# Kernel tuning notes

Hardware: AMD Instinct MI355X
Metric: run time of the kernel (lower is better)

## Reference

```python
import jax, jax.numpy as jnp
import numpy as np

N_NODES = 100000
N_EDGES = 1600000
F_IN, H1, H2, N_CLASSES = 512, 64, 32, 16


def setup_inputs() -> dict:
    key = jax.random.key(0)
    ks = jax.random.split(key, 8)
    glorot = lambda k, fi, fo: jax.random.normal(k, (fi, fo), jnp.float32) * (2.0 / (fi + fo)) ** 0.5
    return {
        "x": jax.random.normal(ks[0], (N_NODES, F_IN), jnp.float32),
        "edge_index": jax.random.randint(ks[1], (2, N_EDGES), 0, N_NODES, jnp.int32),
        "W1": glorot(ks[2], F_IN, H1), "b1": jnp.zeros((H1,), jnp.float32),
        "W2": glorot(ks[3], H1, H2), "b2": jnp.zeros((H2,), jnp.float32),
        "W3": glorot(ks[4], H2, N_CLASSES), "b3": jnp.zeros((N_CLASSES,), jnp.float32),
    }


def _gcn_conv(x, W, b, src, dst, norm, n_nodes):
    # GCNConv: D^{-1/2} (A + I) D^{-1/2} X W + b  (transform-then-propagate)
    h = x @ W                                   # [N, out]
    msg = h[src] * norm[:, None]                # gather + scale, [E', out]
    agg = jax.ops.segment_sum(msg, dst, num_segments=n_nodes)  # scatter-add
    return agg + b


def reference(x, edge_index, W1, b1, W2, b2, W3, b3):
    n = x.shape[0]
    loop = jnp.arange(n, dtype=edge_index.dtype)
    src = jnp.concatenate([edge_index[0], loop])  # add self-loops
    dst = jnp.concatenate([edge_index[1], loop])
    deg = jax.ops.segment_sum(jnp.ones_like(src, dtype=x.dtype), dst, num_segments=n)
    dinv = jnp.where(deg > 0, jax.lax.rsqrt(deg), 0.0)
    norm = dinv[src] * dinv[dst]                  # symmetric normalization per edge

    h = jax.nn.relu(_gcn_conv(x, W1, b1, src, dst, norm, n))
    h = jax.nn.relu(_gcn_conv(h, W2, b2, src, dst, norm, n))  # dropout = identity (eval)
    h = _gcn_conv(h, W3, b3, src, dst, norm, n)
    return jax.nn.log_softmax(h, axis=1)
```

## Files before the change

### kernel.cpp

```cpp
#include <hip/hip_runtime.h>
#include <hip/hip_bf16.h>
#include <cstdint>
#include <cstddef>

#define N_NODES 100000
#define N_EDGES 1600000
#define F_IN 512
#define H1F 64
#define H2F 32
#define NCF 16
#define NB 782
#define NBLK 128
#define CHUNK 12500

typedef __attribute__((ext_vector_type(8))) short bf16x8;
typedef __attribute__((ext_vector_type(8))) unsigned short ushort8;
typedef __attribute__((ext_vector_type(4))) float f32x4;

__device__ inline short f2bf(float f) {
    uint32_t u = __builtin_bit_cast(uint32_t, f);
    return (short)((u + 0x7FFF + ((u >> 16) & 1)) >> 16);
}
__device__ inline float bf2f(unsigned short u) {
    uint32_t x = ((uint32_t)u) << 16;
    return __builtin_bit_cast(float, x);
}

__global__ __launch_bounds__(256) void count_kernel(const int* __restrict__ dst,
                                                    int* __restrict__ mat) {
    __shared__ int lh[NB];
    for (int i = threadIdx.x; i < NB; i += 256) lh[i] = 0;
    __syncthreads();
    int base = blockIdx.x * CHUNK;
    for (int j = base + threadIdx.x; j < base + CHUNK; j += 256)
        atomicAdd(&lh[dst[j] >> 7], 1);
    __syncthreads();
    for (int i = threadIdx.x; i < NB; i += 256)
        mat[blockIdx.x * NB + i] = lh[i];
}

__global__ __launch_bounds__(NBLK) void colscan_kernel(int* __restrict__ mat,
                                                       int* __restrict__ total) {
    __shared__ int s[NBLK];
    int b = blockIdx.x;
    int t = threadIdx.x;
    int v = mat[t * NB + b];
    s[t] = v;
    __syncthreads();
    for (int o = 1; o < NBLK; o <<= 1) {
        int a = (t >= o) ? s[t - o] : 0;
        __syncthreads();
        s[t] += a;
        __syncthreads();
    }
    mat[t * NB + b] = s[t] - v;
    if (t == NBLK - 1) total[b] = s[t];
}

__global__ __launch_bounds__(1024) void bscan_kernel(const int* __restrict__ total,
                                                     int* __restrict__ boff,
                                                     int* __restrict__ row_ptr) {
    __shared__ int s[1024];
    int t = threadIdx.x;
    int v = (t < NB) ? total[t] : 0;
    s[t] = v;
    __syncthreads();
    for (int o = 1; o < 1024; o <<= 1) {
        int a = (t >= o) ? s[t - o] : 0;
        __syncthreads();
        s[t] += a;
        __syncthreads();
    }
    if (t < NB) boff[t] = s[t] - v;
    if (t == 0) {
        boff[NB] = N_EDGES;
        row_ptr[N_NODES] = N_EDGES;
    }
}

__global__ __launch_bounds__(256) void place_kernel(const int* __restrict__ src,
                                                    const int* __restrict__ dst,
                                                    const int* __restrict__ boff,
                                                    const int* __restrict__ mat,
                                                    int* __restrict__ ebuf) {
    __shared__ int lcur[NB];
    for (int i = threadIdx.x; i < NB; i += 256)
        lcur[i] = boff[i] + mat[blockIdx.x * NB + i];
    __syncthreads();
    int base = blockIdx.x * CHUNK;
    for (int j = base + threadIdx.x; j < base + CHUNK; j += 256) {
        int d = dst[j];
        int b = d >> 7;
        int pos = atomicAdd(&lcur[b], 1);
        ebuf[pos] = src[j] | ((d & 127) << 17);
    }
}

__global__ __launch_bounds__(256) void bbuild_kernel(const int* __restrict__ ebuf,
                                                     const int* __restrict__ boff,
                                                     int* __restrict__ row_ptr,
                                                     int* __restrict__ col,
                                                     float* __restrict__ dinv) {
    __shared__ int lcnt[128], lexc[128];
    int b = blockIdx.x;
    int beg = boff[b], end = boff[b + 1];
    int t = threadIdx.x;
    if (t < 128) lcnt[t] = 0;
    __syncthreads();
    for (int j = beg + t; j < end; j += 256)
        atomicAdd(&lcnt[(ebuf[j] >> 17) & 127], 1);
    __syncthreads();
    if (t < 128) lexc[t] = lcnt[t];
    __syncthreads();
    for (int o = 1; o < 128; o <<= 1) {
        int a = (t < 128 && t >= o) ? lexc[t - o] : 0;
        __syncthreads();
        if (t < 128) lexc[t] += a;
        __syncthreads();
    }
    int node0 = b << 7;
    if (t < 128) {
        int n = node0 + t;
        if (n < N_NODES) {
            int ex = lexc[t] - lcnt[t];
            row_ptr[n] = beg + ex;
            dinv[n] = rsqrtf((float)(lcnt[t] + 1));
            lexc[t] = ex;
        }
    }
    __syncthreads();
    for (int j = beg + t; j < end; j += 256) {
        int v = ebuf[j];
        int li = (v >> 17) & 127;
        int p = atomicAdd(&lexc[li], 1);
        col[beg + p] = v & 0x1FFFF;
    }
}

__global__ __launch_bounds__(256) void gemm1_mfma(const float* __restrict__ x,
                                                  const float* __restrict__ W,
                                                  const float* __restrict__ dinv,
                                                  unsigned short* __restrict__ out) {
    __shared__ short As[2][4096];
    __shared__ short Bs[2][2048];
    const int tid = threadIdx.x;
    const int L = tid & 63;
    const int w = tid >> 6;
    const int brow = blockIdx.x * 128;

    f32x4 acc[2][4] = {};

    auto stageA = [&](int kt, int buf) {
        #pragma unroll
        for (int h = 0; h < 2; ++h) {
            int r  = (tid >> 2) + h * 64;
            int kg = tid & 3;
            int gr = brow + r;
            float4 v0 = make_float4(0.f, 0.f, 0.f, 0.f);
            float4 v1 = make_float4(0.f, 0.f, 0.f, 0.f);
            if (gr < N_NODES) {
                const float* p = &x[(size_t)gr * F_IN + kt * 32 + kg * 8];
                v0 = *reinterpret_cast<const float4*>(p);
                v1 = *reinterpret_cast<const float4*>(p + 4);
            }
            short t8[8] = {f2bf(v0.x), f2bf(v0.y), f2bf(v0.z), f2bf(v0.w),
                           f2bf(v1.x), f2bf(v1.y), f2bf(v1.z), f2bf(v1.w)};
            *reinterpret_cast<bf16x8*>(&As[buf][kg * 1024 + (r ^ (kg << 2)) * 8]) =
                *reinterpret_cast<bf16x8*>(t8);
        }
    };
    auto stageB = [&](int kt, int buf) {
        int k0 = kt * 32 + w * 8;
        short t8[8];
        #pragma unroll
        for (int i = 0; i < 8; ++i) t8[i] = f2bf(W[(size_t)(k0 + i) * H1F + L]);
        int byteoff = L * 64 + ((w * 16) ^ ((L & 3) << 4));
        *reinterpret_cast<bf16x8*>((char*)Bs[buf] + byteoff) =
            *reinterpret_cast<bf16x8*>(t8);
    };
    auto compute = [&](int buf) {
        const int kg = L >> 4;
        const int lr = L & 15;
        int r0 = w * 32 + lr;
        int r1 = r0 + 16;
        bf16x8 a0 = *reinterpret_cast<bf16x8*>(&As[buf][kg * 1024 + (r0 ^ (kg << 2)) * 8]);
        bf16x8 a1 = *reinterpret_cast<bf16x8*>(&As[buf][kg * 1024 + (r1 ^ (kg << 2)) * 8]);
        #pragma unroll
        for (int ni = 0; ni < 4; ++ni) {
            int c = ni * 16 + lr;
            bf16x8 b = *reinterpret_cast<bf16x8*>(
                (char*)Bs[buf] + c * 64 + ((kg * 16) ^ ((c & 3) << 4)));
            acc[0][ni] = __builtin_amdgcn_mfma_f32_16x16x32_bf16(a0, b, acc[0][ni], 0, 0, 0);
            acc[1][ni] = __builtin_amdgcn_mfma_f32_16x16x32_bf16(a1, b, acc[1][ni], 0, 0, 0);
        }
    };

    stageA(0, 0);
    stageB(0, 0);
    __syncthreads();
    for (int kt = 0; kt < 16; ++kt) {
        int cur = kt & 1;
        if (kt < 15) {
            stageA(kt + 1, cur ^ 1);
            stageB(kt + 1, cur ^ 1);
        }
        compute(cur);
        __syncthreads();
    }

    #pragma unroll
    for (int mi = 0; mi < 2; ++mi) {
        #pragma unroll
        for (int i = 0; i < 4; ++i) {
            int row = brow + w * 32 + mi * 16 + (L >> 4) * 4 + i;
            if (row < N_NODES) {
                float dv = dinv[row];
                #pragma unroll
                for (int ni = 0; ni < 4; ++ni)
                    out[(size_t)row * H1F + ni * 16 + (L & 15)] =
                        (unsigned short)f2bf(acc[mi][ni][i] * dv);
            }
        }
    }
}

__global__ __launch_bounds__(256) void gemm2_kernel(const unsigned short* __restrict__ h,
                                                    const float* __restrict__ W,
                                                    const float* __restrict__ dinv,
                                                    unsigned short* __restrict__ out) {
    __shared__ float ws[64][32];
    __shared__ float rs[8][64];
    int tid = threadIdx.x;
    int brow = blockIdx.x * 8;
    #pragma unroll
    for (int i = 0; i < 2; ++i) {
        int f = tid + i * 256;
        reinterpret_cast<float4*>(&ws[0][0])[f] = reinterpret_cast<const float4*>(W)[f];
    }
    if (tid < 64) {
        ushort8 v = reinterpret_cast<const ushort8*>(h + (size_t)brow * 64)[tid];
        #pragma unroll
        for (int j = 0; j < 8; ++j) (&rs[0][0])[tid * 8 + j] = bf2f(v[j]);
    }
    __syncthreads();
    int lr = tid >> 5;
    int c = tid & 31;
    float acc = 0.f;
    #pragma unroll
    for (int k = 0; k < 64; ++k) acc += rs[lr][k] * ws[k][c];
    int gr = brow + lr;
    out[(size_t)gr * H2F + c] = (unsigned short)f2bf(acc * dinv[gr]);
}

__global__ __launch_bounds__(256) void gemm3_kernel(const unsigned short* __restrict__ h,
                                                    const float* __restrict__ W,
                                                    const float* __restrict__ dinv,
                                                    unsigned short* __restrict__ out) {
    __shared__ float ws[32][16];
    __shared__ float rs[16][32];
    int tid = threadIdx.x;
    int brow = blockIdx.x * 16;
    if (tid < 128) {
        reinterpret_cast<float4*>(&ws[0][0])[tid] = reinterpret_cast<const float4*>(W)[tid];
    } else if (tid < 192) {
        int t = tid - 128;
        ushort8 v = reinterpret_cast<const ushort8*>(h + (size_t)brow * 32)[t];
        #pragma unroll
        for (int j = 0; j < 8; ++j) (&rs[0][0])[t * 8 + j] = bf2f(v[j]);
    }
    __syncthreads();
    int lr = tid >> 4;
    int c = tid & 15;
    float acc = 0.f;
    #pragma unroll
    for (int k = 0; k < 32; ++k) acc += rs[lr][k] * ws[k][c];
    int gr = brow + lr;
    out[(size_t)gr * NCF + c] = (unsigned short)f2bf(acc * dinv[gr]);
}

template <int F, bool RELU, bool LSM>
__global__ __launch_bounds__(256) void aggregate_kernel(const unsigned short* __restrict__ h,
                                                        const int* __restrict__ row_ptr,
                                                        const int* __restrict__ col,
                                                        const float* __restrict__ dinv,
                                                        const float* __restrict__ bias,
                                                        void* __restrict__ outp) {
    int tid = blockIdx.x * 256 + threadIdx.x;
    int n = tid / F;
    int f = tid % F;
    if (n >= N_NODES) return;
    int beg = row_ptr[n];
    int end = row_ptr[n + 1];
    float sum = bf2f(h[(size_t)n * F + f]);
    int j = beg;
    for (; j + 3 < end; j += 4) {
        int c0 = col[j], c1 = col[j + 1], c2 = col[j + 2], c3 = col[j + 3];
        float s0 = bf2f(h[(size_t)c0 * F + f]);
        float s1 = bf2f(h[(size_t)c1 * F + f]);
        float s2 = bf2f(h[(size_t)c2 * F + f]);
        float s3 = bf2f(h[(size_t)c3 * F + f]);
        sum += (s0 + s1) + (s2 + s3);
    }
    for (; j < end; ++j) sum += bf2f(h[(size_t)col[j] * F + f]);

    float val = sum * dinv[n] + bias[f];
    if (RELU) val = fmaxf(val, 0.f);
    if (LSM) {
        float m = val;
        #pragma unroll
        for (int o = 1; o < F; o <<= 1) m = fmaxf(m, __shfl_xor(m, o));
        float ex = expf(val - m);
        float s = ex;
        #pragma unroll
        for (int o = 1; o < F; o <<= 1) s += __shfl_xor(s, o);
        val = val - m - logf(s);
        ((float*)outp)[(size_t)n * F + f] = val;
    } else {
        ((unsigned short*)outp)[(size_t)n * F + f] = (unsigned short)f2bf(val);
    }
}

extern "C" void kernel_launch(void* const* d_in, const int* in_sizes, int n_in,
                              void* d_out, int out_size, void* d_ws, size_t ws_size,
                              hipStream_t stream) {
    const float* x  = (const float*)d_in[0];
    const int*   ei = (const int*)d_in[1];
    const float* W1 = (const float*)d_in[2];
    const float* b1 = (const float*)d_in[3];
    const float* W2 = (const float*)d_in[4];
    const float* b2 = (const float*)d_in[5];
    const float* W3 = (const float*)d_in[6];
    const float* b3 = (const float*)d_in[7];
    float* out = (float*)d_out;

    const int* src = ei;
    const int* dst = ei + N_EDGES;

    char* ws = (char*)d_ws;
    size_t off = 0;
    auto alloc = [&](size_t bytes) -> void* {
        void* p = ws + off;
        off += (bytes + 255) & ~(size_t)255;
        return p;
    };
    int*            row_ptr = (int*)alloc((size_t)(N_NODES + 1) * 4);
    float*          dinv    = (float*)alloc((size_t)N_NODES * 4);
    int*            col     = (int*)alloc((size_t)N_EDGES * 4);
    unsigned short* bufA    = (unsigned short*)alloc((size_t)N_NODES * 64 * 2);
    unsigned short* bufB    = (unsigned short*)alloc((size_t)N_NODES * 64 * 2);
    int*            mat     = (int*)alloc((size_t)NBLK * NB * 4);
    int*            total   = (int*)alloc((size_t)NB * 4);
    int*            boff    = (int*)alloc((size_t)(NB + 1) * 4);
    int*            ebuf    = (int*)bufA;

    count_kernel<<<NBLK, 256, 0, stream>>>(dst, mat);
    colscan_kernel<<<NB, NBLK, 0, stream>>>(mat, total);
    bscan_kernel<<<1, 1024, 0, stream>>>(total, boff, row_ptr);
    place_kernel<<<NBLK, 256, 0, stream>>>(src, dst, boff, mat, ebuf);
    bbuild_kernel<<<NB, 256, 0, stream>>>(ebuf, boff, row_ptr, col, dinv);

    gemm1_mfma<<<(N_NODES + 127) / 128, 256, 0, stream>>>(x, W1, dinv, bufA);
    aggregate_kernel<64, true, false><<<(N_NODES * 64) / 256, 256, 0, stream>>>(
        bufA, row_ptr, col, dinv, b1, bufB);

    gemm2_kernel<<<N_NODES / 8, 256, 0, stream>>>(bufB, W2, dinv, bufA);
    aggregate_kernel<32, true, false><<<(N_NODES * 32) / 256, 256, 0, stream>>>(
        bufA, row_ptr, col, dinv, b2, bufB);

    gemm3_kernel<<<N_NODES / 16, 256, 0, stream>>>(bufB, W3, dinv, bufA);
    aggregate_kernel<16, false, true><<<(N_NODES * 16) / 256, 256, 0, stream>>>(
        bufA, row_ptr, col, dinv, b3, out);
}
```

Measured before the change: 554.5 us.

## Fuse layer-1/2 aggregation with the next layer's small GEMM

Result: faster. 537.3 us (-3.1%).

```diff
diff --git a/kernel.cpp b/kernel.cpp
--- a/kernel.cpp
+++ b/kernel.cpp
@@ -224,100 +224,122 @@
     }
 }
 
-__global__ __launch_bounds__(256) void gemm2_kernel(const unsigned short* __restrict__ h,
-                                                    const float* __restrict__ W,
-                                                    const float* __restrict__ dinv,
-                                                    unsigned short* __restrict__ out) {
+__global__ __launch_bounds__(256) void agg64_gemm2(const unsigned short* __restrict__ h,
+                                                   const int* __restrict__ row_ptr,
+                                                   const int* __restrict__ col,
+                                                   const float* __restrict__ dinv,
+                                                   const float* __restrict__ b1,
+                                                   const float* __restrict__ W2,
+                                                   unsigned short* __restrict__ out) {
+    __shared__ float zs[4][64];
     __shared__ float ws[64][32];
-    __shared__ float rs[8][64];
     int tid = threadIdx.x;
-    int brow = blockIdx.x * 8;
     #pragma unroll
     for (int i = 0; i < 2; ++i) {
-        int f = tid + i * 256;
-        reinterpret_cast<float4*>(&ws[0][0])[f] = reinterpret_cast<const float4*>(W)[f];
-    }
-    if (tid < 64) {
-        ushort8 v = reinterpret_cast<const ushort8*>(h + (size_t)brow * 64)[tid];
-        #pragma unroll
-        for (int j = 0; j < 8; ++j) (&rs[0][0])[tid * 8 + j] = bf2f(v[j]);
-    }
-    __syncthreads();
-    int lr = tid >> 5;
-    int c = tid & 31;
-    float acc = 0.f;
-    #pragma unroll
-    for (int k = 0; k < 64; ++k) acc += rs[lr][k] * ws[k][c];
-    int gr = brow + lr;
-    out[(size_t)gr * H2F + c] = (unsigned short)f2bf(acc * dinv[gr]);
-}
-
-__global__ __launch_bounds__(256) void gemm3_kernel(const unsigned short* __restrict__ h,
-                                                    const float* __restrict__ W,
-                                                    const float* __restrict__ dinv,
-                                                    unsigned short* __restrict__ out) {
-    __shared__ float ws[32][16];
-    __shared__ float rs[16][32];
-    int tid = threadIdx.x;
-    int brow = blockIdx.x * 16;
-    if (tid < 128) {
-        reinterpret_cast<float4*>(&ws[0][0])[tid] = reinterpret_cast<const float4*>(W)[tid];
-    } else if (tid < 192) {
-        int t = tid - 128;
-        ushort8 v = reinterpret_cast<const ushort8*>(h + (size_t)brow * 32)[t];
-        #pragma unroll
-        for (int j = 0; j < 8; ++j) (&rs[0][0])[t * 8 + j] = bf2f(v[j]);
-    }
-    __syncthreads();
-    int lr = tid >> 4;
-    int c = tid & 15;
-    float acc = 0.f;
-    #pragma unroll
-    for (int k = 0; k < 32; ++k) acc += rs[lr][k] * ws[k][c];
-    int gr = brow + lr;
-    out[(size_t)gr * NCF + c] = (unsigned short)f2bf(acc * dinv[gr]);
-}
-
-template <int F, bool RELU, bool LSM>
-__global__ __launch_bounds__(256) void aggregate_kernel(const unsigned short* __restrict__ h,
-                                                        const int* __restrict__ row_ptr,
-                                                        const int* __restrict__ col,
-                                                        const float* __restrict__ dinv,
-                                                        const float* __restrict__ bias,
-                                                        void* __restrict__ outp) {
-    int tid = blockIdx.x * 256 + threadIdx.x;
-    int n = tid / F;
-    int f = tid % F;
-    if (n >= N_NODES) return;
+        int f4 = tid + i * 256;
+        reinterpret_cast<float4*>(&ws[0][0])[f4] = reinterpret_cast<const float4*>(W2)[f4];
+    }
+    int n = blockIdx.x * 4 + (tid >> 6);
+    int f = tid & 63;
     int beg = row_ptr[n];
     int end = row_ptr[n + 1];
-    float sum = bf2f(h[(size_t)n * F + f]);
+    float sum = bf2f(h[(size_t)n * 64 + f]);
     int j = beg;
     for (; j + 3 < end; j += 4) {
         int c0 = col[j], c1 = col[j + 1], c2 = col[j + 2], c3 = col[j + 3];
-        float s0 = bf2f(h[(size_t)c0 * F + f]);
-        float s1 = bf2f(h[(size_t)c1 * F + f]);
-        float s2 = bf2f(h[(size_t)c2 * F + f]);
-        float s3 = bf2f(h[(size_t)c3 * F + f]);
+        float s0 = bf2f(h[(size_t)c0 * 64 + f]);
+        float s1 = bf2f(h[(size_t)c1 * 64 + f]);
+        float s2 = bf2f(h[(size_t)c2 * 64 + f]);
+        float s3 = bf2f(h[(size_t)c3 * 64 + f]);
         sum += (s0 + s1) + (s2 + s3);
     }
-    for (; j < end; ++j) sum += bf2f(h[(size_t)col[j] * F + f]);
-
-    float val = sum * dinv[n] + bias[f];
-    if (RELU) val = fmaxf(val, 0.f);
-    if (LSM) {
-        float m = val;
-        #pragma unroll
-        for (int o = 1; o < F; o <<= 1) m = fmaxf(m, __shfl_xor(m, o));
-        float ex = expf(val - m);
-        float s = ex;
-        #pragma unroll
-        for (int o = 1; o < F; o <<= 1) s += __shfl_xor(s, o);
-        val = val - m - logf(s);
-        ((float*)outp)[(size_t)n * F + f] = val;
-    } else {
-        ((unsigned short*)outp)[(size_t)n * F + f] = (unsigned short)f2bf(val);
-    }
+    for (; j < end; ++j) sum += bf2f(h[(size_t)col[j] * 64 + f]);
+    float val = fmaxf(sum * dinv[n] + b1[f], 0.f);
+    zs[tid >> 6][f] = val;
+    __syncthreads();
+    if (tid < 128) {
+        int ln = tid >> 5;
+        int c = tid & 31;
+        float acc = 0.f;
+        #pragma unroll
+        for (int k = 0; k < 64; ++k) acc += zs[ln][k] * ws[k][c];
+        int gn = blockIdx.x * 4 + ln;
+        out[(size_t)gn * H2F + c] = (unsigned short)f2bf(acc * dinv[gn]);
+    }
+}
+
+__global__ __launch_bounds__(256) void agg32_gemm3(const unsigned short* __restrict__ h,
+                                                   const int* __restrict__ row_ptr,
+                                                   const int* __restrict__ col,
+                                                   const float* __restrict__ dinv,
+                                                   const float* __restrict__ b2,
+                                                   const float* __restrict__ W3,
+                                                   unsigned short* __restrict__ out) {
+    __shared__ float zs[8][32];
+    __shared__ float ws[32][16];
+    int tid = threadIdx.x;
+    if (tid < 128)
+        reinterpret_cast<float4*>(&ws[0][0])[tid] = reinterpret_cast<const float4*>(W3)[tid];
+    int n = blockIdx.x * 8 + (tid >> 5);
+    int f = tid & 31;
+    int beg = row_ptr[n];
+    int end = row_ptr[n + 1];
+    float sum = bf2f(h[(size_t)n * 32 + f]);
+    int j = beg;
+    for (; j + 3 < end; j += 4) {
+        int c0 = col[j], c1 = col[j + 1], c2 = col[j + 2], c3 = col[j + 3];
+        float s0 = bf2f(h[(size_t)c0 * 32 + f]);
+        float s1 = bf2f(h[(size_t)c1 * 32 + f]);
+        float s2 = bf2f(h[(size_t)c2 * 32 + f]);
+        float s3 = bf2f(h[(size_t)c3 * 32 + f]);
+        sum += (s0 + s1) + (s2 + s3);
+    }
+    for (; j < end; ++j) sum += bf2f(h[(size_t)col[j] * 32 + f]);
+    float val = fmaxf(sum * dinv[n] + b2[f], 0.f);
+    zs[tid >> 5][f] = val;
+    __syncthreads();
+    if (tid < 128) {
+        int ln = tid >> 4;
+        int c = tid & 15;
+        float acc = 0.f;
+        #pragma unroll
+        for (int k = 0; k < 32; ++k) acc += zs[ln][k] * ws[k][c];
+        int gn = blockIdx.x * 8 + ln;
+        out[(size_t)gn * NCF + c] = (unsigned short)f2bf(acc * dinv[gn]);
+    }
+}
+
+__global__ __launch_bounds__(256) void agg16_lsm(const unsigned short* __restrict__ h,
+                                                 const int* __restrict__ row_ptr,
+                                                 const int* __restrict__ col,
+                                                 const float* __restrict__ dinv,
+                                                 const float* __restrict__ b3,
+                                                 float* __restrict__ out) {
+    int tid = blockIdx.x * 256 + threadIdx.x;
+    int n = tid / NCF;
+    int f = tid % NCF;
+    int beg = row_ptr[n];
+    int end = row_ptr[n + 1];
+    float sum = bf2f(h[(size_t)n * NCF + f]);
+    int j = beg;
+    for (; j + 3 < end; j += 4) {
+        int c0 = col[j], c1 = col[j + 1], c2 = col[j + 2], c3 = col[j + 3];
+        float s0 = bf2f(h[(size_t)c0 * NCF + f]);
+        float s1 = bf2f(h[(size_t)c1 * NCF + f]);
+        float s2 = bf2f(h[(size_t)c2 * NCF + f]);
+        float s3 = bf2f(h[(size_t)c3 * NCF + f]);
+        sum += (s0 + s1) + (s2 + s3);
+    }
+    for (; j < end; ++j) sum += bf2f(h[(size_t)col[j] * NCF + f]);
+    float val = sum * dinv[n] + b3[f];
+    float m = val;
+    #pragma unroll
+    for (int o = 1; o < NCF; o <<= 1) m = fmaxf(m, __shfl_xor(m, o));
+    float ex = expf(val - m);
+    float s = ex;
+    #pragma unroll
+    for (int o = 1; o < NCF; o <<= 1) s += __shfl_xor(s, o);
+    out[(size_t)n * NCF + f] = val - m - logf(s);
 }
 
 extern "C" void kernel_launch(void* const* d_in, const int* in_sizes, int n_in,
@@ -347,7 +369,8 @@
     float*          dinv    = (float*)alloc((size_t)N_NODES * 4);
     int*            col     = (int*)alloc((size_t)N_EDGES * 4);
     unsigned short* bufA    = (unsigned short*)alloc((size_t)N_NODES * 64 * 2);
-    unsigned short* bufB    = (unsigned short*)alloc((size_t)N_NODES * 64 * 2);
+    unsigned short* bufB    = (unsigned short*)alloc((size_t)N_NODES * 32 * 2);
+    unsigned short* bufC    = (unsigned short*)alloc((size_t)N_NODES * 16 * 2);
     int*            mat     = (int*)alloc((size_t)NBLK * NB * 4);
     int*            total   = (int*)alloc((size_t)NB * 4);
     int*            boff    = (int*)alloc((size_t)(NB + 1) * 4);
@@ -360,14 +383,7 @@
     bbuild_kernel<<<NB, 256, 0, stream>>>(ebuf, boff, row_ptr, col, dinv);
 
     gemm1_mfma<<<(N_NODES + 127) / 128, 256, 0, stream>>>(x, W1, dinv, bufA);
-    aggregate_kernel<64, true, false><<<(N_NODES * 64) / 256, 256, 0, stream>>>(
-        bufA, row_ptr, col, dinv, b1, bufB);
-
-    gemm2_kernel<<<N_NODES / 8, 256, 0, stream>>>(bufB, W2, dinv, bufA);
-    aggregate_kernel<32, true, false><<<(N_NODES * 32) / 256, 256, 0, stream>>>(
-        bufA, row_ptr, col, dinv, b2, bufB);
-
-    gemm3_kernel<<<N_NODES / 16, 256, 0, stream>>>(bufB, W3, dinv, bufA);
-    aggregate_kernel<16, false, true><<<(N_NODES * 16) / 256, 256, 0, stream>>>(
-        bufA, row_ptr, col, dinv, b3, out);
-}
+    agg64_gemm2<<<N_NODES / 4, 256, 0, stream>>>(bufA, row_ptr, col, dinv, b1, W2, bufB);
+    agg32_gemm3<<<N_NODES / 8, 256, 0, stream>>>(bufB, row_ptr, col, dinv, b2, W3, bufC);
+    agg16_lsm<<<(N_NODES * NCF) / 256, 256, 0, stream>>>(bufC, row_ptr, col, dinv, b3, out);
+}
```
